# Optimization experiments

Hardware: AMD Instinct MI355X
Metric: run time of the kernel (lower is better)

Reference implementation:

```python
import jax, jax.numpy as jnp
import numpy as np

B, Fc, C, H, D, L = 128, 256, 256, 8, 32, 6  # batch, columns, dim, heads, head_dim, layers


def _ln(x, g, b, eps=1e-5):
    m = x.mean(-1, keepdims=True)
    v = ((x - m) ** 2).mean(-1, keepdims=True)
    return (x - m) * jax.lax.rsqrt(v + eps) * g + b


def setup_inputs() -> dict:
    key = jax.random.key(0)
    ks = jax.random.split(key, 16)
    s = 0.02  # weight init scale to keep 6-layer activations stable
    return {
        "x": jax.random.normal(ks[0], (B, Fc, C), jnp.float32),
        "col_emb": jax.random.normal(ks[1], (1, Fc, C), jnp.float32),
        "pos_emb": jax.random.normal(ks[2], (1, Fc + 1, C), jnp.float32),
        "col_bias": jax.random.normal(ks[3], (Fc, Fc), jnp.float32),
        "ln1_g": jnp.ones((L, C), jnp.float32),
        "ln1_b": jnp.zeros((L, C), jnp.float32),
        "qkv_w": jax.random.normal(ks[4], (L, C, 3 * C), jnp.float32) * s,
        "qkv_b": jnp.zeros((L, 3 * C), jnp.float32),
        "out_w": jax.random.normal(ks[5], (L, C, C), jnp.float32) * s,
        "out_b": jnp.zeros((L, C), jnp.float32),
        "ln2_g": jnp.ones((L, C), jnp.float32),
        "ln2_b": jnp.zeros((L, C), jnp.float32),
        "w1": jax.random.normal(ks[6], (L, C, 4 * C), jnp.float32) * s,
        "b1": jnp.zeros((L, 4 * C), jnp.float32),
        "w2": jax.random.normal(ks[7], (L, 4 * C, 2 * C), jnp.float32) * s,
        "b2": jnp.zeros((L, 2 * C), jnp.float32),
        "w3": jax.random.normal(ks[8], (L, C, C), jnp.float32) * s,
        "b3": jnp.zeros((L, C), jnp.float32),
        "fin_g": jnp.ones((C,), jnp.float32),
        "fin_b": jnp.zeros((C,), jnp.float32),
    }


def reference(x, col_emb, pos_emb, col_bias, ln1_g, ln1_b, qkv_w, qkv_b,
              out_w, out_b, ln2_g, ln2_b, w1, b1, w2, b2, w3, b3, fin_g, fin_b):
    Fdim = x.shape[1]
    h = x + col_emb[:, :Fdim] + pos_emb[:, 1:Fdim + 1]
    bias = col_bias[:Fdim, :Fdim]  # [T, T]
    scale = 1.0 / np.sqrt(D).astype(np.float32)
    params = (ln1_g, ln1_b, qkv_w, qkv_b, out_w, out_b, ln2_g, ln2_b,
              w1, b1, w2, b2, w3, b3)

    def block(xc, p):
        g1, be1, qw, qb, ow, ob, g2, be2, W1, B1, W2, B2, W3, B3 = p
        Bn, T, Cd = xc.shape
        hn = _ln(xc, g1, be1)
        qkv = hn @ qw + qb                              # [B,T,3C]
        q, k, v = jnp.split(qkv, 3, axis=-1)
        q = q.reshape(Bn, T, H, D)
        k = k.reshape(Bn, T, H, D)
        v = v.reshape(Bn, T, H, D)
        scores = jnp.einsum('bthd,bshd->bhts', q, k) * scale + bias[None, None]
        w = jax.nn.softmax(scores, axis=-1)             # dropout = identity (eval)
        attn = jnp.einsum('bhts,bshd->bthd', w, v).reshape(Bn, T, Cd)
        attn = attn @ ow + ob
        attn = attn + bias[None]                        # [1,T,T] broadcast, T==C
        xc = xc + attn
        hn2 = _ln(xc, g2, be2)
        u = jax.nn.gelu(hn2 @ W1 + B1, approximate=False)
        gl = u @ W2 + B2                                # [B,T,2C]
        a, gate = jnp.split(gl, 2, axis=-1)
        xc = xc + (a * jax.nn.sigmoid(gate)) @ W3 + B3
        return xc, None

    h, _ = jax.lax.scan(block, h, params)
    h = _ln(h, fin_g, fin_b)
    return h.mean(axis=1)  # pooling='mean' -> [B, C]
```

## Files before the change

### kernel.cpp

```cpp
#include <hip/hip_runtime.h>

typedef __bf16 bx8 __attribute__((ext_vector_type(8)));
typedef float fx4 __attribute__((ext_vector_type(4)));

#define GAS(p) ((const __attribute__((address_space(1))) void*)(const void*)(p))
#define LAS(p) ((__attribute__((address_space(3))) void*)(void*)(p))

__device__ __forceinline__ unsigned short f2bf(float f) {
  return __builtin_bit_cast(unsigned short, (__bf16)f);
}
__device__ __forceinline__ float bf2f(unsigned short s) {
  unsigned u = ((unsigned)s) << 16;
  return __builtin_bit_cast(float, u);
}

__global__ __launch_bounds__(256) void wtrans_kernel(const float* __restrict__ src,
                                                     unsigned short* __restrict__ dst,
                                                     int K, int N) {
  __shared__ unsigned short t[64][68];
  const int l = blockIdx.z;
  const float* s = src + (size_t)l * K * N;
  unsigned short* d = dst + (size_t)l * N * K;
  const int n0 = blockIdx.x * 64, k0 = blockIdx.y * 64;
  const int tx = threadIdx.x & 63, ty = threadIdx.x >> 6;
#pragma unroll
  for (int r = 0; r < 64; r += 4)
    t[tx][ty + r] = f2bf(s[(size_t)(k0 + ty + r) * N + n0 + tx]);
  __syncthreads();
#pragma unroll
  for (int r = 0; r < 64; r += 4)
    d[(size_t)(n0 + ty + r) * K + k0 + tx] = t[ty + r][tx];
}

__global__ __launch_bounds__(256) void embed_kernel(const float4* __restrict__ x,
                                                    const float4* __restrict__ ce,
                                                    const float4* __restrict__ pe,
                                                    float4* __restrict__ o) {
  int i = blockIdx.x * 256 + threadIdx.x;
  int c4 = i & 63;
  int t = (i >> 6) & 255;
  float4 a = x[i], b = ce[t * 64 + c4], p = pe[(t + 1) * 64 + c4];
  o[i] = make_float4(a.x + b.x + p.x, a.y + b.y + p.y, a.z + b.z + p.z, a.w + b.w + p.w);
}

template <int MODE>
__global__ __launch_bounds__(256) void ln_kernel(const float* __restrict__ x,
                                                 const float* __restrict__ gw,
                                                 const float* __restrict__ bw,
                                                 unsigned short* __restrict__ out,
                                                 float2* __restrict__ stats) {
  int row = blockIdx.x * 4 + (threadIdx.x >> 6);
  int lane = threadIdx.x & 63;
  const float4 v = *(const float4*)(x + (size_t)row * 256 + lane * 4);
  float s = v.x + v.y + v.z + v.w;
  float q = v.x * v.x + v.y * v.y + v.z * v.z + v.w * v.w;
#pragma unroll
  for (int off = 1; off < 64; off <<= 1) {
    s += __shfl_xor(s, off);
    q += __shfl_xor(q, off);
  }
  float mean = s * (1.0f / 256.0f);
  float rs = rsqrtf(q * (1.0f / 256.0f) - mean * mean + 1e-5f);
  if (MODE == 1) {
    if (lane == 0) stats[row] = make_float2(mean, rs);
    return;
  }
  float4 gv = *(const float4*)(gw + lane * 4);
  float4 bv = *(const float4*)(bw + lane * 4);
  ushort4 o;
  o.x = f2bf((v.x - mean) * rs * gv.x + bv.x);
  o.y = f2bf((v.y - mean) * rs * gv.y + bv.y);
  o.z = f2bf((v.z - mean) * rs * gv.z + bv.z);
  o.w = f2bf((v.w - mean) * rs * gv.w + bv.w);
  *(ushort4*)(out + (size_t)row * 256 + lane * 4) = o;
}

__global__ __launch_bounds__(256) void mean_part_kernel(const float* __restrict__ x,
                                                        const float2* __restrict__ stats,
                                                        float* __restrict__ part) {
  int b = blockIdx.x, half = blockIdx.y, c = threadIdx.x;
  const float* xb = x + (size_t)b * 65536 + half * 32768;
  const float2* st = stats + b * 256 + half * 128;
  float acc = 0.f;
#pragma unroll 4
  for (int t = 0; t < 128; ++t) {
    float2 s = st[t];
    acc += (xb[t * 256 + c] - s.x) * s.y;
  }
  part[(size_t)(b * 2 + half) * 256 + c] = acc;
}
__global__ __launch_bounds__(256) void mean_fin_kernel(const float* __restrict__ part,
                                                       const float* __restrict__ fg,
                                                       const float* __restrict__ fb,
                                                       float* __restrict__ out) {
  int b = blockIdx.x, c = threadIdx.x;
  out[b * 256 + c] =
      (part[(size_t)(2 * b) * 256 + c] + part[(size_t)(2 * b + 1) * 256 + c]) *
          (1.0f / 256.0f) * fg[c] + fb[c];
}

template <int EP>
__global__ __launch_bounds__(256) void gemm_kernel(const unsigned short* __restrict__ A,
                                                   const unsigned short* __restrict__ BT,
                                                   const float* __restrict__ bvec,
                                                   const float* __restrict__ cbias,
                                                   float* __restrict__ resid,
                                                   unsigned short* __restrict__ outb,
                                                   int N, int K) {
  __shared__ unsigned short lA[2][128 * 32];
  __shared__ unsigned short lB[2][128 * 32];
  const int tid = threadIdx.x;
  const int lane = tid & 63, w = tid >> 6;
  const int wr = w >> 1, wc = w & 1;
  const int g = lane >> 4, lr = lane & 15;
  const int m0 = blockIdx.y * 128, n0 = blockIdx.x * 128;
  fx4 acc[4][4] = {};

  auto STAGE = [&](int buf, int kk) {
#pragma unroll
    for (int r = 0; r < 2; ++r) {
      int u = r * 256 + tid;
      int row = u >> 2, sl = u & 3;
      int c = sl ^ ((row >> 1) & 3);
      __builtin_amdgcn_global_load_lds(GAS(A + (size_t)(m0 + row) * K + kk + c * 8),
                                       LAS(&lA[buf][u * 8]), 16, 0, 0);
      __builtin_amdgcn_global_load_lds(GAS(BT + (size_t)(n0 + row) * K + kk + c * 8),
                                       LAS(&lB[buf][u * 8]), 16, 0, 0);
    }
  };
  auto COMPUTE = [&](int buf) {
    bx8 af[4], bq[4];
#pragma unroll
    for (int i = 0; i < 4; ++i) {
      int row = wr * 64 + i * 16 + lr;
      af[i] = *(const bx8*)&lA[buf][row * 32 + (g ^ ((row >> 1) & 3)) * 8];
      int col = wc * 64 + i * 16 + lr;
      bq[i] = *(const bx8*)&lB[buf][col * 32 + (g ^ ((col >> 1) & 3)) * 8];
    }
#pragma unroll
    for (int i = 0; i < 4; ++i)
#pragma unroll
      for (int j = 0; j < 4; ++j)
        acc[i][j] = __builtin_amdgcn_mfma_f32_16x16x32_bf16(bq[j], af[i], acc[i][j], 0, 0, 0);
  };

  STAGE(0, 0);
  asm volatile("s_waitcnt vmcnt(0)" ::: "memory");
  __syncthreads();
  int cur = 0;
  const int nt = K >> 5;
  for (int t2 = 1; t2 < nt; ++t2) {
    STAGE(cur ^ 1, t2 * 32);
    COMPUTE(cur);
    __syncthreads();
    cur ^= 1;
  }
  COMPUTE(cur);

#pragma unroll
  for (int i = 0; i < 4; ++i) {
    const int m = m0 + wr * 64 + i * 16 + lr;
#pragma unroll
    for (int j = 0; j < 4; ++j) {
      const int nc = n0 + wc * 64 + j * 16 + g * 4;
      const float4 bv = *(const float4*)(bvec + nc);
      float v0 = acc[i][j][0] + bv.x, v1 = acc[i][j][1] + bv.y;
      float v2 = acc[i][j][2] + bv.z, v3 = acc[i][j][3] + bv.w;
      if constexpr (EP == 1) {
        v0 = 0.5f * v0 * (1.0f + erff(v0 * 0.70710678118654752f));
        v1 = 0.5f * v1 * (1.0f + erff(v1 * 0.70710678118654752f));
        v2 = 0.5f * v2 * (1.0f + erff(v2 * 0.70710678118654752f));
        v3 = 0.5f * v3 * (1.0f + erff(v3 * 0.70710678118654752f));
      }
      if constexpr (EP == 0 || EP == 1) {
        ushort4 st;
        st.x = f2bf(v0); st.y = f2bf(v1); st.z = f2bf(v2); st.w = f2bf(v3);
        *(ushort4*)(outb + (size_t)m * N + nc) = st;
      } else {
        if (nc < 512) {
          ushort4 st;
          st.x = f2bf(v0); st.y = f2bf(v1); st.z = f2bf(v2); st.w = f2bf(v3);
          *(ushort4*)(outb + (size_t)m * N + nc) = st;
        } else {
          unsigned short* vTp = (unsigned short*)resid;
          const int s = m & 255, b = m >> 8;
          const int hv = nc - 512;
          const int h = hv >> 5, d0 = hv & 31;
          const int jj = (s & 3) + 4 * ((s >> 4) & 1);
          const int ub = (s >> 5) * 128 + ((s >> 2) & 3) * 32 + d0;
          unsigned short* base = vTp + (size_t)(b * 8 + h) * 8192;
          const float vv[4] = {v0, v1, v2, v3};
#pragma unroll
          for (int r = 0; r < 4; ++r) {
            int u = ub + r;
            int up = (u & ~7) | ((u & 7) ^ ((u >> 3) & 7));
            base[up * 8 + jj] = f2bf(vv[r]);
          }
        }
      }
    }
  }
}

template <int EP>
__global__ __launch_bounds__(256) void gemm64_kernel(const unsigned short* __restrict__ A,
                                                     const unsigned short* __restrict__ BT,
                                                     const float* __restrict__ bvec,
                                                     const float* __restrict__ cbias,
                                                     float* __restrict__ resid,
                                                     int N, int K) {
  __shared__ unsigned short lA[2][64 * 32];
  __shared__ unsigned short lB[2][128 * 32];
  const int tid = threadIdx.x;
  const int lane = tid & 63, w = tid >> 6;
  const int g = lane >> 4, lr = lane & 15;
  const int m0 = blockIdx.y * 64, n0 = blockIdx.x * 128;
  fx4 acc[4][2] = {};

  auto STAGE = [&](int buf, int kk) {
    {
      int u = tid;
      int row = u >> 2, sl = u & 3;
      int c = sl ^ ((row >> 1) & 3);
      __builtin_amdgcn_global_load_lds(GAS(A + (size_t)(m0 + row) * K + kk + c * 8),
                                       LAS(&lA[buf][u * 8]), 16, 0, 0);
    }
#pragma unroll
    for (int r = 0; r < 2; ++r) {
      int u = r * 256 + tid;
      int row = u >> 2, sl = u & 3;
      int c = sl ^ ((row >> 1) & 3);
      __builtin_amdgcn_global_load_lds(GAS(BT + (size_t)(n0 + row) * K + kk + c * 8),
                                       LAS(&lB[buf][u * 8]), 16, 0, 0);
    }
  };
  auto COMPUTE = [&](int buf) {
    bx8 af[4], bq[2];
#pragma unroll
    for (int i = 0; i < 4; ++i) {
      int row = i * 16 + lr;
      af[i] = *(const bx8*)&lA[buf][row * 32 + (g ^ ((row >> 1) & 3)) * 8];
    }
#pragma unroll
    for (int j = 0; j < 2; ++j) {
      int col = w * 32 + j * 16 + lr;
      bq[j] = *(const bx8*)&lB[buf][col * 32 + (g ^ ((col >> 1) & 3)) * 8];
    }
#pragma unroll
    for (int i = 0; i < 4; ++i)
#pragma unroll
      for (int j = 0; j < 2; ++j)
        acc[i][j] = __builtin_amdgcn_mfma_f32_16x16x32_bf16(bq[j], af[i], acc[i][j], 0, 0, 0);
  };

  STAGE(0, 0);
  asm volatile("s_waitcnt vmcnt(0)" ::: "memory");
  __syncthreads();
  int cur = 0;
  const int nt = K >> 5;
  for (int t2 = 1; t2 < nt; ++t2) {
    STAGE(cur ^ 1, t2 * 32);
    COMPUTE(cur);
    __syncthreads();
    cur ^= 1;
  }
  COMPUTE(cur);

#pragma unroll
  for (int i = 0; i < 4; ++i) {
    const int m = m0 + i * 16 + lr;
#pragma unroll
    for (int j = 0; j < 2; ++j) {
      const int nc = n0 + w * 32 + j * 16 + g * 4;
      const float4 bv = *(const float4*)(bvec + nc);
      float v0 = acc[i][j][0] + bv.x, v1 = acc[i][j][1] + bv.y;
      float v2 = acc[i][j][2] + bv.z, v3 = acc[i][j][3] + bv.w;
      if constexpr (EP == 2) {
        const float4 cb = *(const float4*)(cbias + (size_t)(m & 255) * 256 + nc);
        v0 += cb.x; v1 += cb.y; v2 += cb.z; v3 += cb.w;
      }
      float4* rp = (float4*)(resid + (size_t)m * N + nc);
      float4 old = *rp;
      *rp = make_float4(old.x + v0, old.y + v1, old.z + v2, old.w + v3);
    }
  }
}

__global__ __launch_bounds__(256) void gemm_w2f64_kernel(const unsigned short* __restrict__ A,
                                                         const unsigned short* __restrict__ BT,
                                                         const float* __restrict__ b2,
                                                         unsigned short* __restrict__ gout) {
  __shared__ unsigned short lA[2][64 * 32];
  __shared__ unsigned short lBa[2][128 * 32];
  __shared__ unsigned short lBg[2][128 * 32];
  const int tid = threadIdx.x;
  const int lane = tid & 63, w = tid >> 6;
  const int g = lane >> 4, lr = lane & 15;
  const int m0 = blockIdx.y * 64, n0 = blockIdx.x * 128;
  fx4 aA[4][2] = {}, aG[4][2] = {};

  auto STAGE = [&](int buf, int kk) {
    {
      int u = tid;
      int row = u >> 2, sl = u & 3;
      int c = sl ^ ((row >> 1) & 3);
      __builtin_amdgcn_global_load_lds(GAS(A + (size_t)(m0 + row) * 1024 + kk + c * 8),
                                       LAS(&lA[buf][u * 8]), 16, 0, 0);
    }
#pragma unroll
    for (int r = 0; r < 2; ++r) {
      int u = r * 256 + tid;
      int row = u >> 2, sl = u & 3;
      int c = sl ^ ((row >> 1) & 3);
      __builtin_amdgcn_global_load_lds(GAS(BT + (size_t)(n0 + row) * 1024 + kk + c * 8),
                                       LAS(&lBa[buf][u * 8]), 16, 0, 0);
      __builtin_amdgcn_global_load_lds(GAS(BT + (size_t)(256 + n0 + row) * 1024 + kk + c * 8),
                                       LAS(&lBg[buf][u * 8]), 16, 0, 0);
    }
  };
  auto COMPUTE = [&](int buf) {
    bx8 af[4], ba[2], bg[2];
#pragma unroll
    for (int i = 0; i < 4; ++i) {
      int row = i * 16 + lr;
      af[i] = *(const bx8*)&lA[buf][row * 32 + (g ^ ((row >> 1) & 3)) * 8];
    }
#pragma unroll
    for (int j = 0; j < 2; ++j) {
      int col = w * 32 + j * 16 + lr;
      int sw = (g ^ ((col >> 1) & 3)) * 8;
      ba[j] = *(const bx8*)&lBa[buf][col * 32 + sw];
      bg[j] = *(const bx8*)&lBg[buf][col * 32 + sw];
    }
#pragma unroll
    for (int i = 0; i < 4; ++i)
#pragma unroll
      for (int j = 0; j < 2; ++j) {
        aA[i][j] = __builtin_amdgcn_mfma_f32_16x16x32_bf16(ba[j], af[i], aA[i][j], 0, 0, 0);
        aG[i][j] = __builtin_amdgcn_mfma_f32_16x16x32_bf16(bg[j], af[i], aG[i][j], 0, 0, 0);
      }
  };

  STAGE(0, 0);
  asm volatile("s_waitcnt vmcnt(0)" ::: "memory");
  __syncthreads();
  int cur = 0;
  for (int t2 = 1; t2 < 32; ++t2) {
    STAGE(cur ^ 1, t2 * 32);
    COMPUTE(cur);
    __syncthreads();
    cur ^= 1;
  }
  COMPUTE(cur);

#pragma unroll
  for (int i = 0; i < 4; ++i) {
    const int m = m0 + i * 16 + lr;
#pragma unroll
    for (int j = 0; j < 2; ++j) {
      const int nc = n0 + w * 32 + j * 16 + g * 4;
      const float4 bva = *(const float4*)(b2 + nc);
      const float4 bvg = *(const float4*)(b2 + 256 + nc);
      float a0 = aA[i][j][0] + bva.x, a1 = aA[i][j][1] + bva.y;
      float a2 = aA[i][j][2] + bva.z, a3 = aA[i][j][3] + bva.w;
      float g0 = aG[i][j][0] + bvg.x, g1 = aG[i][j][1] + bvg.y;
      float g2 = aG[i][j][2] + bvg.z, g3 = aG[i][j][3] + bvg.w;
      ushort4 st;
      st.x = f2bf(a0 / (1.0f + __expf(-g0)));
      st.y = f2bf(a1 / (1.0f + __expf(-g1)));
      st.z = f2bf(a2 / (1.0f + __expf(-g2)));
      st.w = f2bf(a3 / (1.0f + __expf(-g3)));
      *(ushort4*)(gout + (size_t)m * 256 + nc) = st;
    }
  }
}

__global__ __launch_bounds__(256) void attn_kernel(const unsigned short* __restrict__ qkv,
                                                   const unsigned short* __restrict__ vT,
                                                   const float* __restrict__ cbias,
                                                   unsigned short* __restrict__ attnb) {
  __shared__ unsigned short Kl[256 * 32];
  __shared__ unsigned short Vl[1024 * 8];
  const int bh = blockIdx.x, b = bh >> 3, h = bh & 7;
  const int tid = threadIdx.x, lane = tid & 63, w = tid >> 6;
  const int g = lane >> 4, lr = lane & 15;
  const unsigned short* qb_ = qkv + (size_t)b * 196608;
  const unsigned short* vTb = vT + (size_t)bh * 8192;
#pragma unroll
  for (int r = 0; r < 4; ++r) {
    int u = r * 256 + tid;
    int s = u >> 2, sl = u & 3;
    int c = sl ^ ((s >> 1) & 3);
    __builtin_amdgcn_global_load_lds(GAS(qb_ + (size_t)s * 768 + 256 + h * 32 + c * 8),
                                     LAS(&Kl[u * 8]), 16, 0, 0);
    __builtin_amdgcn_global_load_lds(GAS(vTb + u * 8), LAS(&Vl[u * 8]), 16, 0, 0);
  }
  asm volatile("s_waitcnt vmcnt(0)" ::: "memory");
  __syncthreads();
  const float scale = 0.17677669529663689f;
  const fx4 zero = {0.f, 0.f, 0.f, 0.f};
#pragma unroll 1
  for (int it = 0; it < 4; ++it) {
    const int t = it * 64 + w * 16 + lr;
    bx8 qf = *(const bx8*)(qb_ + (size_t)t * 768 + h * 32 + g * 8);
    float p[16][4];
    float mx = -1e30f;
#pragma unroll
    for (int n = 0; n < 16; ++n) {
      int sr = n * 16 + lr;
      bx8 kf = *(const bx8*)&Kl[sr * 32 + (g ^ ((sr >> 1) & 3)) * 8];
      fx4 sc = __builtin_amdgcn_mfma_f32_16x16x32_bf16(kf, qf, zero, 0, 0, 0);
      const float4 cb = *(const float4*)(cbias + (size_t)t * 256 + n * 16 + g * 4);
      p[n][0] = sc[0] * scale + cb.x;
      p[n][1] = sc[1] * scale + cb.y;
      p[n][2] = sc[2] * scale + cb.z;
      p[n][3] = sc[3] * scale + cb.w;
      mx = fmaxf(mx, fmaxf(fmaxf(p[n][0], p[n][1]), fmaxf(p[n][2], p[n][3])));
    }
    mx = fmaxf(mx, __shfl_xor(mx, 16));
    mx = fmaxf(mx, __shfl_xor(mx, 32));
    float sum = 0.f;
    bx8 bq[8];
#pragma unroll
    for (int c = 0; c < 8; ++c) {
      union { bx8 v; unsigned short u[8]; } pk;
#pragma unroll
      for (int jj = 0; jj < 8; ++jj) {
        float e = __expf(p[2 * c + (jj >> 2)][jj & 3] - mx);
        sum += e;
        pk.u[jj] = f2bf(e);
      }
      bq[c] = pk.v;
    }
    sum += __shfl_xor(sum, 16);
    sum += __shfl_xor(sum, 32);
    const float inv = 1.0f / sum;
    fx4 oa0 = zero, oa1 = zero;
#pragma unroll
    for (int c = 0; c < 8; ++c) {
      int u0 = c * 128 + g * 32 + lr;
      int u0p = (u0 & ~7) | ((u0 & 7) ^ ((u0 >> 3) & 7));
      bx8 vf0 = *(const bx8*)&Vl[u0p * 8];
      oa0 = __builtin_amdgcn_mfma_f32_16x16x32_bf16(vf0, bq[c], oa0, 0, 0, 0);
      int u1 = u0 + 16;
      int u1p = (u1 & ~7) | ((u1 & 7) ^ ((u1 >> 3) & 7));
      bx8 vf1 = *(const bx8*)&Vl[u1p * 8];
      oa1 = __builtin_amdgcn_mfma_f32_16x16x32_bf16(vf1, bq[c], oa1, 0, 0, 0);
    }
    ushort4 o0, o1;
    o0.x = f2bf(oa0[0] * inv); o0.y = f2bf(oa0[1] * inv);
    o0.z = f2bf(oa0[2] * inv); o0.w = f2bf(oa0[3] * inv);
    o1.x = f2bf(oa1[0] * inv); o1.y = f2bf(oa1[1] * inv);
    o1.z = f2bf(oa1[2] * inv); o1.w = f2bf(oa1[3] * inv);
    unsigned short* orow = attnb + (size_t)(b * 256 + t) * 256 + h * 32;
    *(ushort4*)(orow + 4 * g) = o0;
    *(ushort4*)(orow + 16 + 4 * g) = o1;
  }
}

extern "C" void kernel_launch(void* const* d_in, const int* in_sizes, int n_in,
                              void* d_out, int out_size, void* d_ws, size_t ws_size,
                              hipStream_t stream) {
  (void)in_sizes; (void)n_in; (void)out_size; (void)ws_size;
  const float* x     = (const float*)d_in[0];
  const float* cemb  = (const float*)d_in[1];
  const float* pemb  = (const float*)d_in[2];
  const float* cbias = (const float*)d_in[3];
  const float* ln1g  = (const float*)d_in[4];
  const float* ln1b  = (const float*)d_in[5];
  const float* qkvw  = (const float*)d_in[6];
  const float* qkvb  = (const float*)d_in[7];
  const float* outw  = (const float*)d_in[8];
  const float* outbv = (const float*)d_in[9];
  const float* ln2g  = (const float*)d_in[10];
  const float* ln2b  = (const float*)d_in[11];
  const float* w1    = (const float*)d_in[12];
  const float* b1    = (const float*)d_in[13];
  const float* w2    = (const float*)d_in[14];
  const float* b2    = (const float*)d_in[15];
  const float* w3    = (const float*)d_in[16];
  const float* b3    = (const float*)d_in[17];
  const float* fing  = (const float*)d_in[18];
  const float* finb  = (const float*)d_in[19];

  char* ws = (char*)d_ws;
  float* x_res = (float*)(ws);
  unsigned short* hn   = (unsigned short*)(ws + 33554432);
  unsigned short* big  = (unsigned short*)(ws + 50331648);
  unsigned short* vT   = (unsigned short*)(ws + 100663296);
  unsigned short* wT   = (unsigned short*)(ws + 117440512);
  float2* stats = (float2*)(ws + 130809856);
  float* part  = (float*)big;

  unsigned short* qkvwT = wT;
  unsigned short* outwT = wT + 1179648;
  unsigned short* w1T   = wT + 1572864;
  unsigned short* w2T   = wT + 3145728;
  unsigned short* w3T   = wT + 6291456;

  wtrans_kernel<<<dim3(12, 4, 6), 256, 0, stream>>>(qkvw, qkvwT, 256, 768);
  wtrans_kernel<<<dim3(4, 4, 6), 256, 0, stream>>>(outw, outwT, 256, 256);
  wtrans_kernel<<<dim3(16, 4, 6), 256, 0, stream>>>(w1, w1T, 256, 1024);
  wtrans_kernel<<<dim3(8, 16, 6), 256, 0, stream>>>(w2, w2T, 1024, 512);
  wtrans_kernel<<<dim3(4, 4, 6), 256, 0, stream>>>(w3, w3T, 256, 256);
  embed_kernel<<<8192, 256, 0, stream>>>((const float4*)x, (const float4*)cemb,
                                         (const float4*)pemb, (float4*)x_res);
  for (int l = 0; l < 6; ++l) {
    ln_kernel<0><<<8192, 256, 0, stream>>>(x_res, ln1g + l * 256, ln1b + l * 256, hn, nullptr);
    gemm_kernel<4><<<dim3(6, 256), 256, 0, stream>>>(hn, qkvwT + (size_t)l * 196608,
                                                     qkvb + l * 768, nullptr, (float*)vT,
                                                     big, 768, 256);
    attn_kernel<<<1024, 256, 0, stream>>>(big, vT, cbias, hn);
    gemm64_kernel<2><<<dim3(2, 512), 256, 0, stream>>>(hn, outwT + (size_t)l * 65536,
                                                       outbv + l * 256, cbias, x_res,
                                                       256, 256);
    ln_kernel<0><<<8192, 256, 0, stream>>>(x_res, ln2g + l * 256, ln2b + l * 256, hn, nullptr);
    gemm_kernel<1><<<dim3(8, 256), 256, 0, stream>>>(hn, w1T + (size_t)l * 262144,
                                                     b1 + l * 1024, nullptr, nullptr, big,
                                                     1024, 256);
    gemm_w2f64_kernel<<<dim3(2, 512), 256, 0, stream>>>(big, w2T + (size_t)l * 524288,
                                                        b2 + l * 512, hn);
    gemm64_kernel<3><<<dim3(2, 512), 256, 0, stream>>>(hn, w3T + (size_t)l * 65536,
                                                       b3 + l * 256, nullptr, x_res,
                                                       256, 256);
  }
  ln_kernel<1><<<8192, 256, 0, stream>>>(x_res, nullptr, nullptr, nullptr, stats);
  mean_part_kernel<<<dim3(128, 2), 256, 0, stream>>>(x_res, stats, part);
  mean_fin_kernel<<<128, 256, 0, stream>>>(part, fing, finb, (float*)d_out);
}
```

Before: 1.571 ms.

## Prefetch two K-tiles ahead in GEMM kernels with fine-grained vmcnt waits

Restructures the main loops of the three GEMM kernels so two K-tiles are staged up front. Each iteration waits only on the oldest outstanding global-to-LDS loads using counted vmcnt values instead of draining all loads. After the fragments are read into registers, the freed LDS buffer is refilled for tile t+2 before the MFMAs run, so loads overlap compute for longer. The cost is two barriers per iteration and hand-tuned vmcnt counts that must match the number of loads each STAGE issues.

```diff
diff --git a/kernel.cpp b/kernel.cpp
--- a/kernel.cpp
+++ b/kernel.cpp
@@ -5,6 +5,10 @@
 
 #define GAS(p) ((const __attribute__((address_space(1))) void*)(const void*)(p))
 #define LAS(p) ((__attribute__((address_space(3))) void*)(void*)(p))
+#define WAITVM(n) do { asm volatile("s_waitcnt vmcnt(" #n ")" ::: "memory"); \
+                       __builtin_amdgcn_sched_barrier(0); } while (0)
+#define WAITLG0() do { asm volatile("s_waitcnt lgkmcnt(0)" ::: "memory"); \
+                       __builtin_amdgcn_sched_barrier(0); } while (0)
 
 __device__ __forceinline__ unsigned short f2bf(float f) {
   return __builtin_bit_cast(unsigned short, (__bf16)f);
@@ -128,7 +132,14 @@
                                        LAS(&lB[buf][u * 8]), 16, 0, 0);
     }
   };
-  auto COMPUTE = [&](int buf) {
+
+  const int nt = K >> 5;
+  STAGE(0, 0);
+  STAGE(1, 32);
+  for (int t = 0; t < nt; ++t) {
+    if (t == nt - 1) WAITVM(0); else WAITVM(4);
+    __builtin_amdgcn_s_barrier();
+    const int buf = t & 1;
     bx8 af[4], bq[4];
 #pragma unroll
     for (int i = 0; i < 4; ++i) {
@@ -137,25 +148,15 @@
       int col = wc * 64 + i * 16 + lr;
       bq[i] = *(const bx8*)&lB[buf][col * 32 + (g ^ ((col >> 1) & 3)) * 8];
     }
+    WAITLG0();
+    __builtin_amdgcn_s_barrier();
+    if (t + 2 < nt) STAGE(buf, (t + 2) * 32);
 #pragma unroll
     for (int i = 0; i < 4; ++i)
 #pragma unroll
       for (int j = 0; j < 4; ++j)
         acc[i][j] = __builtin_amdgcn_mfma_f32_16x16x32_bf16(bq[j], af[i], acc[i][j], 0, 0, 0);
-  };
-
-  STAGE(0, 0);
-  asm volatile("s_waitcnt vmcnt(0)" ::: "memory");
-  __syncthreads();
-  int cur = 0;
-  const int nt = K >> 5;
-  for (int t2 = 1; t2 < nt; ++t2) {
-    STAGE(cur ^ 1, t2 * 32);
-    COMPUTE(cur);
-    __syncthreads();
-    cur ^= 1;
-  }
-  COMPUTE(cur);
+  }
 
 #pragma unroll
   for (int i = 0; i < 4; ++i) {
@@ -234,7 +235,14 @@
                                        LAS(&lB[buf][u * 8]), 16, 0, 0);
     }
   };
-  auto COMPUTE = [&](int buf) {
+
+  const int nt = K >> 5;
+  STAGE(0, 0);
+  STAGE(1, 32);
+  for (int t = 0; t < nt; ++t) {
+    if (t == nt - 1) WAITVM(0); else WAITVM(3);
+    __builtin_amdgcn_s_barrier();
+    const int buf = t & 1;
     bx8 af[4], bq[2];
 #pragma unroll
     for (int i = 0; i < 4; ++i) {
@@ -246,25 +254,15 @@
       int col = w * 32 + j * 16 + lr;
       bq[j] = *(const bx8*)&lB[buf][col * 32 + (g ^ ((col >> 1) & 3)) * 8];
     }
+    WAITLG0();
+    __builtin_amdgcn_s_barrier();
+    if (t + 2 < nt) STAGE(buf, (t + 2) * 32);
 #pragma unroll
     for (int i = 0; i < 4; ++i)
 #pragma unroll
       for (int j = 0; j < 2; ++j)
         acc[i][j] = __builtin_amdgcn_mfma_f32_16x16x32_bf16(bq[j], af[i], acc[i][j], 0, 0, 0);
-  };
-
-  STAGE(0, 0);
-  asm volatile("s_waitcnt vmcnt(0)" ::: "memory");
-  __syncthreads();
-  int cur = 0;
-  const int nt = K >> 5;
-  for (int t2 = 1; t2 < nt; ++t2) {
-    STAGE(cur ^ 1, t2 * 32);
-    COMPUTE(cur);
-    __syncthreads();
-    cur ^= 1;
-  }
-  COMPUTE(cur);
+  }
 
 #pragma unroll
   for (int i = 0; i < 4; ++i) {
@@ -318,7 +316,13 @@
                                        LAS(&lBg[buf][u * 8]), 16, 0, 0);
     }
   };
-  auto COMPUTE = [&](int buf) {
+
+  STAGE(0, 0);
+  STAGE(1, 32);
+  for (int t = 0; t < 32; ++t) {
+    if (t == 31) WAITVM(0); else WAITVM(5);
+    __builtin_amdgcn_s_barrier();
+    const int buf = t & 1;
     bx8 af[4], ba[2], bg[2];
 #pragma unroll
     for (int i = 0; i < 4; ++i) {
@@ -332,6 +336,9 @@
       ba[j] = *(const bx8*)&lBa[buf][col * 32 + sw];
       bg[j] = *(const bx8*)&lBg[buf][col * 32 + sw];
     }
+    WAITLG0();
+    __builtin_amdgcn_s_barrier();
+    if (t + 2 < 32) STAGE(buf, (t + 2) * 32);
 #pragma unroll
     for (int i = 0; i < 4; ++i)
 #pragma unroll
@@ -339,19 +346,7 @@
         aA[i][j] = __builtin_amdgcn_mfma_f32_16x16x32_bf16(ba[j], af[i], aA[i][j], 0, 0, 0);
         aG[i][j] = __builtin_amdgcn_mfma_f32_16x16x32_bf16(bg[j], af[i], aG[i][j], 0, 0, 0);
       }
-  };
-
-  STAGE(0, 0);
-  asm volatile("s_waitcnt vmcnt(0)" ::: "memory");
-  __syncthreads();
-  int cur = 0;
-  for (int t2 = 1; t2 < 32; ++t2) {
-    STAGE(cur ^ 1, t2 * 32);
-    COMPUTE(cur);
-    __syncthreads();
-    cur ^= 1;
-  }
-  COMPUTE(cur);
+  }
 
 #pragma unroll
   for (int i = 0; i < 4; ++i) {
```

After: 1.540 ms. 2.0% less time.
